# Optimization experiments

Measured on AMD Instinct MI355X. Metric: run time of the kernel, lower is better.

## Reference

```python
import jax, jax.numpy as jnp
import numpy as np

E = 1024          # embd_size
HS = 64           # head_size
NH = E // HS      # num heads = 16
B, T = 2, 2048


def setup_inputs() -> dict:
    key = jax.random.key(0)
    ks = jax.random.split(key, 9)
    s = 1.0 / np.sqrt(E)
    inp = {
        "embd_q": jax.random.normal(ks[0], (B, T, E), dtype=jnp.float32),
        # torch nn.Linear weights are [out, in]; y = x @ W.T + b
        "Wq": jax.random.uniform(ks[1], (E, E), jnp.float32, -s, s),
        "bq": jax.random.uniform(ks[2], (E,), jnp.float32, -s, s),
        "Wk": jax.random.uniform(ks[3], (E, E), jnp.float32, -s, s),
        "bk": jax.random.uniform(ks[4], (E,), jnp.float32, -s, s),
        "Wv": jax.random.uniform(ks[5], (E, E), jnp.float32, -s, s),
        "bv": jax.random.uniform(ks[6], (E,), jnp.float32, -s, s),
        "Wo": jax.random.uniform(ks[7], (E, E), jnp.float32, -s, s),
        "bo": jax.random.uniform(ks[8], (E,), jnp.float32, -s, s),
    }
    return inp


def reference(embd_q, Wq, bq, Wk, bk, Wv, bv, Wo, bo):
    b, t, e = embd_q.shape
    q = embd_q @ Wq.T + bq
    k = embd_q @ Wk.T + bk
    v = embd_q @ Wv.T + bv
    # [B, NH, T, HS]
    q = q.reshape(b, t, NH, HS).transpose(0, 2, 1, 3)
    k = k.reshape(b, t, NH, HS).transpose(0, 2, 1, 3)
    v = v.reshape(b, t, NH, HS).transpose(0, 2, 1, 3)
    w = jnp.einsum("bhqd,bhkd->bhqk", q, k) / jnp.sqrt(jnp.float32(HS))
    causal = jnp.triu(jnp.ones((t, t), dtype=bool), k=1)  # True above diag
    w = jnp.where(causal[None, None, :, :], -jnp.inf, w)
    w = jax.nn.softmax(w, axis=-1)
    a = jnp.einsum("bhqk,bhkd->bhqd", w, v)
    a = a.transpose(0, 2, 1, 3).reshape(b, t, e)
    return a @ Wo.T + bo
```

## Files before the change

### kernel.cpp

```cpp
#include <hip/hip_runtime.h>

typedef unsigned short u16;
typedef __bf16 bf16x8 __attribute__((ext_vector_type(8)));
typedef __bf16 bf16x4 __attribute__((ext_vector_type(4)));
typedef __bf16 bf16x2 __attribute__((ext_vector_type(2)));
typedef short s16x4 __attribute__((ext_vector_type(4)));
typedef float f32x4 __attribute__((ext_vector_type(4)));

#define Mdim 4096
#define Ndim 1024
#define Kdim 1024

__device__ __forceinline__ u16 f2bf(float f) {
    unsigned u = __float_as_uint(f);
    u += 0x7FFF + ((u >> 16) & 1);
    return (u16)(u >> 16);
}

__device__ __forceinline__ void gl_lds16(const u16* g, u16* l) {
    __builtin_amdgcn_global_load_lds(
        (const __attribute__((address_space(1))) unsigned int*)g,
        (__attribute__((address_space(3))) unsigned int*)l, 16, 0, 0);
}

__device__ __forceinline__ f32x4 mfma16(s16x4 a, s16x4 b, f32x4 c) {
#if __has_builtin(__builtin_amdgcn_mfma_f32_16x16x16_bf16)
    return __builtin_amdgcn_mfma_f32_16x16x16_bf16(
        __builtin_bit_cast(bf16x4, a), __builtin_bit_cast(bf16x4, b), c, 0, 0, 0);
#else
    return __builtin_amdgcn_mfma_f32_16x16x16bf16_1k(a, b, c, 0, 0, 0);
#endif
}

#if __has_builtin(__builtin_amdgcn_exp2f)
#define EXP2(x) __builtin_amdgcn_exp2f(x)
#else
#define EXP2(x) exp2f(x)
#endif

__device__ __forceinline__ s16x4 pack4bf(float a, float b, float c, float d) {
#if __has_builtin(__builtin_amdgcn_cvt_pk_bf16_f32)
    union { struct { bf16x2 lo, hi; } v; s16x4 s; } u;
    u.v.lo = __builtin_amdgcn_cvt_pk_bf16_f32(a, b);
    u.v.hi = __builtin_amdgcn_cvt_pk_bf16_f32(c, d);
    return u.s;
#else
    s16x4 r;
    r.x = (short)f2bf(a); r.y = (short)f2bf(b);
    r.z = (short)f2bf(c); r.w = (short)f2bf(d);
    return r;
#endif
}

__global__ __launch_bounds__(256) void cast_all(
    const float* __restrict__ X,
    const float* __restrict__ Wq, const float* __restrict__ Wk,
    const float* __restrict__ Wv, const float* __restrict__ Wo,
    u16* __restrict__ Xb,
    u16* __restrict__ Wqb, u16* __restrict__ Wkb,
    u16* __restrict__ Wvb, u16* __restrict__ Wob) {
    size_t i4 = (size_t)blockIdx.x * blockDim.x + threadIdx.x;
    size_t flat = i4 * 4;
    const float* src;
    u16* dst;
    size_t off;
    if (flat < (size_t)4194304) {
        src = X; dst = Xb; off = flat;
    } else {
        size_t r = flat - 4194304;
        int w = (int)(r >> 20);
        off = r & 1048575;
        src = (w == 0) ? Wq : (w == 1) ? Wk : (w == 2) ? Wv : Wo;
        dst = (w == 0) ? Wqb : (w == 1) ? Wkb : (w == 2) ? Wvb : Wob;
    }
    float4 v = *(const float4*)(src + off);
    ushort4 o;
    o.x = f2bf(v.x); o.y = f2bf(v.y); o.z = f2bf(v.z); o.w = f2bf(v.w);
    *(ushort4*)(dst + off) = o;
}

template <int BN>
__device__ __forceinline__ void gemm_core(const u16* __restrict__ A,
                                          const u16* __restrict__ Bw,
                                          const float* __restrict__ bias,
                                          void* __restrict__ out,
                                          int n0, int mode) {
    __shared__ __align__(16) u16 At[128 * 64];
    __shared__ __align__(16) u16 Bt[BN * 64];
    const int tid = threadIdx.x, w = tid >> 6, lane = tid & 63;
    const int quad = lane >> 4, l16 = lane & 15;
    const int wm = w & 1, wn = w >> 1;
    const int m0 = blockIdx.x * 128;
    constexpr int NTN = BN / 32;
    f32x4 acc[4][NTN] = {};
    const int r8 = lane >> 3, c8 = lane & 7;

    for (int k0 = 0; k0 < Kdim; k0 += 64) {
        __syncthreads();
#pragma unroll
        for (int i = 0; i < 4; ++i) {
            int row = w * 32 + i * 8 + r8;
            int j = c8 ^ (row & 7);
            gl_lds16(A + (size_t)(m0 + row) * Kdim + k0 + j * 8,
                     &At[(w * 32 + i * 8) * 64]);
        }
#pragma unroll
        for (int i = 0; i < BN / 32; ++i) {
            int row = w * (BN / 4) + i * 8 + r8;
            int j = c8 ^ (row & 7);
            gl_lds16(Bw + (size_t)(n0 + row) * Kdim + k0 + j * 8,
                     &Bt[(w * (BN / 4) + i * 8) * 64]);
        }
        __syncthreads();
#pragma unroll
        for (int ks = 0; ks < 2; ++ks) {
            bf16x8 af[4], bf[NTN];
#pragma unroll
            for (int mt = 0; mt < 4; ++mt) {
                int r = wm * 64 + mt * 16 + l16;
                af[mt] = *(const bf16x8*)&At[r * 64 + ((ks * 4 + quad) ^ (r & 7)) * 8];
            }
#pragma unroll
            for (int nt = 0; nt < NTN; ++nt) {
                int r = wn * (BN / 2) + nt * 16 + l16;
                bf[nt] = *(const bf16x8*)&Bt[r * 64 + ((ks * 4 + quad) ^ (r & 7)) * 8];
            }
#pragma unroll
            for (int mt = 0; mt < 4; ++mt)
#pragma unroll
                for (int nt = 0; nt < NTN; ++nt)
                    acc[mt][nt] = __builtin_amdgcn_mfma_f32_16x16x32_bf16(
                        af[mt], bf[nt], acc[mt][nt], 0, 0, 0);
        }
    }

#pragma unroll
    for (int nt = 0; nt < NTN; ++nt) {
        int n = n0 + wn * (BN / 2) + nt * 16 + l16;
        float bb = bias[n];
        const int h = n >> 6, d = n & 63;
        const int ksf = (d >> 5) & 1, quadf8 = (d >> 3) & 3, jj = d & 7;
        const int dtf = d >> 4, l16f = d & 15;
#pragma unroll
        for (int mt = 0; mt < 4; ++mt) {
            int mbase = m0 + wm * 64 + mt * 16 + quad * 4;
            if (mode == 2) {
                int b = mbase >> 11, t = mbase & 2047;
                int kt = t >> 5, kl = t & 31;
                int c = kl >> 4, quadf = (kl >> 2) & 3;
                ushort4 pk;
                pk.x = f2bf(acc[mt][nt][0] + bb);
                pk.y = f2bf(acc[mt][nt][1] + bb);
                pk.z = f2bf(acc[mt][nt][2] + bb);
                pk.w = f2bf(acc[mt][nt][3] + bb);
                *(ushort4*)&((u16*)out)[(size_t)(b * 16 + h) * 131072 + kt * 2048 +
                                        (c * 4 + dtf) * 256 + (quadf * 16 + l16f) * 4] = pk;
            } else if (mode == 3 || mode == 4) {
#pragma unroll
                for (int r = 0; r < 4; ++r) {
                    int m = mbase + r;
                    int b = m >> 11, t = m & 2047;
                    int blk = t >> 5, tl = t & 31;
                    int cq = tl >> 4, l16q = tl & 15;
                    ((u16*)out)[(size_t)(b * 16 + h) * 131072 + blk * 2048 +
                                (cq * 2 + ksf) * 512 + (quadf8 * 16 + l16q) * 8 + jj] =
                        f2bf(acc[mt][nt][r] + bb);
                }
            } else {
#pragma unroll
                for (int r = 0; r < 4; ++r)
                    ((float*)out)[(size_t)(mbase + r) * Ndim + n] = acc[mt][nt][r] + bb;
            }
        }
    }
}

__global__ __launch_bounds__(256, 2) void qkv_gemm(
    const u16* __restrict__ Xb,
    const u16* __restrict__ Wqb, const u16* __restrict__ Wkb, const u16* __restrict__ Wvb,
    const float* __restrict__ bq, const float* __restrict__ bk, const float* __restrict__ bv,
    u16* __restrict__ Qw, u16* __restrict__ Kw, u16* __restrict__ Vw) {
    const int y = blockIdx.y;
    const int z = y >> 3;
    const int n0 = (y & 7) * 128;
    const u16* Bw = (z == 0) ? Wqb : (z == 1) ? Wkb : Wvb;
    const float* bias = (z == 0) ? bq : (z == 1) ? bk : bv;
    void* out = (z == 0) ? (void*)Qw : (z == 1) ? (void*)Kw : (void*)Vw;
    gemm_core<128>(Xb, Bw, bias, out, n0, (z == 0) ? 3 : (z == 1) ? 4 : 2);
}

__global__ __launch_bounds__(256, 2) void out_gemm(
    const u16* __restrict__ Aatt, const u16* __restrict__ Wob,
    const float* __restrict__ bo, float* __restrict__ out) {
    gemm_core<64>(Aatt, Wob, bo, out, blockIdx.y * 64, 1);
}

__global__ __launch_bounds__(256, 3) void flash_attn(
    const u16* __restrict__ QF, const u16* __restrict__ KF,
    const u16* __restrict__ VF, u16* __restrict__ Aatt) {
    __shared__ float oLds[4 * 2112];
    __shared__ float lsumLds[4][32];

    const int tid = threadIdx.x, w = tid >> 6, lane = tid & 63;
    const int quad = lane >> 4, l16 = lane & 15;
    const int g = blockIdx.x;
    const int bh = g & 31;
    const int strip = 63 - (g >> 5);
    const int qbase = strip * 32;
    const int ntw = strip + 1;

    const u16* QFh = QF + (size_t)bh * 131072;
    const u16* KFh = KF + (size_t)bh * 131072;
    const u16* VFh = VF + (size_t)bh * 131072;
    const int b = bh >> 4, h = bh & 15;
    const float c1 = 0.18033688011112042f;

    bf16x8 qf[2][2];
#pragma unroll
    for (int qt = 0; qt < 2; ++qt)
#pragma unroll
        for (int ks = 0; ks < 2; ++ks)
            qf[qt][ks] = *(const bf16x8*)(QFh + (size_t)strip * 2048 +
                                          (qt * 2 + ks) * 512 + lane * 8);

    f32x4 o[2][4] = {};
    float lsum[2] = {0.f, 0.f};

#define LOADT(kt_, ka_, vf_)                                                   \
    {                                                                          \
        const u16* kp_ = KFh + (size_t)(kt_) * 2048;                           \
        const u16* vp_ = VFh + (size_t)(kt_) * 2048;                           \
        _Pragma("unroll")                                                      \
        for (int c_ = 0; c_ < 2; ++c_) {                                       \
            _Pragma("unroll")                                                  \
            for (int ks_ = 0; ks_ < 2; ++ks_)                                  \
                ka_[c_][ks_] = *(const bf16x8*)(kp_ + (c_ * 2 + ks_) * 512     \
                                                + lane * 8);                   \
            _Pragma("unroll")                                                  \
            for (int dt_ = 0; dt_ < 4; ++dt_)                                  \
                vf_[c_][dt_] = *(const s16x4*)(vp_ + (c_ * 4 + dt_) * 256      \
                                               + lane * 4);                    \
        }                                                                      \
    }

#define COMPUTE(kt_, ka_, vf_)                                                 \
    {                                                                          \
        const bool dm_ = ((kt_) == ntw - 1);                                   \
        _Pragma("unroll")                                                      \
        for (int c_ = 0; c_ < 2; ++c_) {                                       \
            _Pragma("unroll")                                                  \
            for (int qt_ = 0; qt_ < 2; ++qt_) {                                \
                f32x4 z_ = {};                                                 \
                z_ = __builtin_amdgcn_mfma_f32_16x16x32_bf16(                  \
                    ka_[c_][0], qf[qt_][0], z_, 0, 0, 0);                      \
                z_ = __builtin_amdgcn_mfma_f32_16x16x32_bf16(                  \
                    ka_[c_][1], qf[qt_][1], z_, 0, 0, 0);                      \
                float p_[4];                                                   \
                if (dm_) {                                                     \
                    int q_ = qbase + qt_ * 16 + l16;                           \
                    int kkb_ = (kt_) * 32 + c_ * 16 + quad * 4;                \
                    _Pragma("unroll")                                          \
                    for (int r_ = 0; r_ < 4; ++r_)                             \
                        p_[r_] = (kkb_ + r_ > q_) ? 0.f : EXP2(z_[r_] * c1);   \
                } else {                                                       \
                    _Pragma("unroll")                                          \
                    for (int r_ = 0; r_ < 4; ++r_) p_[r_] = EXP2(z_[r_] * c1); \
                }                                                              \
                lsum[qt_] += (p_[0] + p_[1]) + (p_[2] + p_[3]);                \
                s16x4 pa_ = pack4bf(p_[0], p_[1], p_[2], p_[3]);               \
                _Pragma("unroll")                                              \
                for (int dt_ = 0; dt_ < 4; ++dt_)                              \
                    o[qt_][dt_] = mfma16(pa_, vf_[c_][dt_], o[qt_][dt_]);      \
            }                                                                  \
        }                                                                      \
    }

    bf16x8 kaA[2][2], kaB[2][2];
    s16x4 vfA[2][4], vfB[2][4];
    int kt = w;
    if (kt < ntw) {
        LOADT(kt, kaA, vfA);
        while (true) {
            int nx = kt + 4;
            if (nx < ntw) {
                LOADT(nx, kaB, vfB);
                asm volatile("s_waitcnt vmcnt(12)" ::: "memory");
            } else {
                asm volatile("s_waitcnt vmcnt(0)" ::: "memory");
            }
            COMPUTE(kt, kaA, vfA);
            kt = nx;
            if (kt >= ntw) break;
            nx = kt + 4;
            if (nx < ntw) {
                LOADT(nx, kaA, vfA);
                asm volatile("s_waitcnt vmcnt(12)" ::: "memory");
            } else {
                asm volatile("s_waitcnt vmcnt(0)" ::: "memory");
            }
            COMPUTE(kt, kaB, vfB);
            kt = nx;
            if (kt >= ntw) break;
        }
    }

#pragma unroll
    for (int qt = 0; qt < 2; ++qt) {
        float l = lsum[qt];
        l += __shfl_xor(l, 16);
        l += __shfl_xor(l, 32);
        if (lane < 16) lsumLds[w][qt * 16 + lane] = l;
#pragma unroll
        for (int dt = 0; dt < 4; ++dt)
#pragma unroll
            for (int r = 0; r < 4; ++r)
                oLds[w * 2112 + (qt * 16 + quad * 4 + r) * 66 + dt * 16 + l16] =
                    o[qt][dt][r];
    }
    __syncthreads();
    {
        const int q = tid >> 3, dd = (tid & 7) * 8;
        float l = lsumLds[0][q] + lsumLds[1][q] + lsumLds[2][q] + lsumLds[3][q];
        float inv = 1.0f / l;
        f32x4 a0 = {}, a1 = {};
#pragma unroll
        for (int ww = 0; ww < 4; ++ww) {
            a0 += *(const f32x4*)&oLds[ww * 2112 + q * 66 + dd];
            a1 += *(const f32x4*)&oLds[ww * 2112 + q * 66 + dd + 4];
        }
        const int t = qbase + q;
        ushort4 p0, p1;
        p0.x = f2bf(a0[0] * inv); p0.y = f2bf(a0[1] * inv);
        p0.z = f2bf(a0[2] * inv); p0.w = f2bf(a0[3] * inv);
        p1.x = f2bf(a1[0] * inv); p1.y = f2bf(a1[1] * inv);
        p1.z = f2bf(a1[2] * inv); p1.w = f2bf(a1[3] * inv);
        u16* dst = Aatt + ((size_t)(b * 2048 + t)) * 1024 + h * 64 + dd;
        *(ushort4*)dst = p0;
        *(ushort4*)(dst + 4) = p1;
    }
}

extern "C" void kernel_launch(void* const* d_in, const int* in_sizes, int n_in,
                              void* d_out, int out_size, void* d_ws, size_t ws_size,
                              hipStream_t stream) {
    const float* X  = (const float*)d_in[0];
    const float* Wq = (const float*)d_in[1];
    const float* bq = (const float*)d_in[2];
    const float* Wk = (const float*)d_in[3];
    const float* bk = (const float*)d_in[4];
    const float* Wv = (const float*)d_in[5];
    const float* bv = (const float*)d_in[6];
    const float* Wo = (const float*)d_in[7];
    const float* bo = (const float*)d_in[8];

    char* ws = (char*)d_ws;
    const size_t MB = 1 << 20;
    u16* Xb   = (u16*)(ws);
    u16* Wqb  = (u16*)(ws + 8  * MB);
    u16* Wkb  = (u16*)(ws + 10 * MB);
    u16* Wvb  = (u16*)(ws + 12 * MB);
    u16* Wob  = (u16*)(ws + 14 * MB);
    u16* Qw   = (u16*)(ws + 16 * MB);
    u16* Kw   = (u16*)(ws + 24 * MB);
    u16* Vw   = (u16*)(ws + 32 * MB);
    u16* Aatt = (u16*)(ws + 40 * MB);

    cast_all<<<8192, 256, 0, stream>>>(X, Wq, Wk, Wv, Wo, Xb, Wqb, Wkb, Wvb, Wob);
    qkv_gemm<<<dim3(32, 24), 256, 0, stream>>>(Xb, Wqb, Wkb, Wvb, bq, bk, bv, Qw, Kw, Vw);
    flash_attn<<<dim3(2048), 256, 0, stream>>>(Qw, Kw, Vw, Aatt);
    out_gemm<<<dim3(32, 16), 256, 0, stream>>>(Aatt, Wob, bo, (float*)d_out);
}
```

Baseline: 167.4 us.

## Pre-swizzle operands into MFMA fragment layout and give each attention wave its own strip

The cast kernel now writes X, Wq, Wk and Wv directly in MFMA fragment order, so the QKV GEMM loads fragments straight from global memory into registers with double buffering and no LDS or barriers. Flash attention changes from four waves splitting the key tiles of one query strip (reduced through LDS) to each wave owning a separate query strip over all its keys. This removes the cross-wave reduction and shrinks the grid from 2048 to 512 blocks. The cost is that causal work is uneven across the four waves of a block, and output stores become scalar 16-bit writes.

Result: slower. 190.0 us (+13.4%).

```diff
diff --git a/kernel.cpp b/kernel.cpp
--- a/kernel.cpp
+++ b/kernel.cpp
@@ -52,91 +52,105 @@
 #endif
 }
 
-__global__ __launch_bounds__(256) void cast_all(
+__global__ __launch_bounds__(256) void cast_swz(
     const float* __restrict__ X,
     const float* __restrict__ Wq, const float* __restrict__ Wk,
     const float* __restrict__ Wv, const float* __restrict__ Wo,
-    u16* __restrict__ Xb,
-    u16* __restrict__ Wqb, u16* __restrict__ Wkb,
-    u16* __restrict__ Wvb, u16* __restrict__ Wob) {
-    size_t i4 = (size_t)blockIdx.x * blockDim.x + threadIdx.x;
-    size_t flat = i4 * 4;
+    u16* __restrict__ Xf,
+    u16* __restrict__ Wqf, u16* __restrict__ Wkf,
+    u16* __restrict__ Wvf, u16* __restrict__ Wob) {
+    size_t flat = ((size_t)blockIdx.x * 256 + threadIdx.x) * 8;
     const float* src;
     u16* dst;
-    size_t off;
-    if (flat < (size_t)4194304) {
-        src = X; dst = Xb; off = flat;
+    size_t soff;
+    int row = 0, col = 0;
+    bool frag;
+    if (flat < 4194304) {
+        src = X; dst = Xf; soff = flat;
+        row = (int)(flat >> 10); col = (int)(flat & 1023); frag = true;
     } else {
         size_t r = flat - 4194304;
-        int w = (int)(r >> 20);
-        off = r & 1048575;
-        src = (w == 0) ? Wq : (w == 1) ? Wk : (w == 2) ? Wv : Wo;
-        dst = (w == 0) ? Wqb : (w == 1) ? Wkb : (w == 2) ? Wvb : Wob;
-    }
-    float4 v = *(const float4*)(src + off);
-    ushort4 o;
-    o.x = f2bf(v.x); o.y = f2bf(v.y); o.z = f2bf(v.z); o.w = f2bf(v.w);
-    *(ushort4*)(dst + off) = o;
-}
-
-template <int BN>
-__device__ __forceinline__ void gemm_core(const u16* __restrict__ A,
-                                          const u16* __restrict__ Bw,
-                                          const float* __restrict__ bias,
-                                          void* __restrict__ out,
-                                          int n0, int mode) {
-    __shared__ __align__(16) u16 At[128 * 64];
-    __shared__ __align__(16) u16 Bt[BN * 64];
+        if (r < 3145728) {
+            int wsel = (int)(r >> 20);
+            soff = r & 1048575;
+            src = (wsel == 0) ? Wq : (wsel == 1) ? Wk : Wv;
+            dst = (wsel == 0) ? Wqf : (wsel == 1) ? Wkf : Wvf;
+            row = (int)(soff >> 10); col = (int)(soff & 1023); frag = true;
+        } else {
+            soff = r - 3145728;
+            src = Wo; dst = Wob; frag = false;
+        }
+    }
+    float4 v0 = *(const float4*)(src + soff);
+    float4 v1 = *(const float4*)(src + soff + 4);
+    u16 t[8];
+    t[0] = f2bf(v0.x); t[1] = f2bf(v0.y); t[2] = f2bf(v0.z); t[3] = f2bf(v0.w);
+    t[4] = f2bf(v1.x); t[5] = f2bf(v1.y); t[6] = f2bf(v1.z); t[7] = f2bf(v1.w);
+    size_t doff = frag
+        ? ((((size_t)(row >> 4) * 32 + (col >> 5)) * 4 + ((col >> 3) & 3)) * 128
+           + (size_t)(row & 15) * 8)
+        : soff;
+    *(uint4*)(dst + doff) = *(uint4*)t;
+}
+
+__global__ __launch_bounds__(256, 3) void qkv_gemm(
+    const u16* __restrict__ Xf,
+    const u16* __restrict__ Wqf, const u16* __restrict__ Wkf, const u16* __restrict__ Wvf,
+    const float* __restrict__ bq, const float* __restrict__ bk, const float* __restrict__ bv,
+    u16* __restrict__ Qw, u16* __restrict__ Kw, u16* __restrict__ Vw) {
+    const int y = blockIdx.y;
+    const int z = y >> 3;
+    const int n0 = (y & 7) * 128;
+    const u16* Wf = (z == 0) ? Wqf : (z == 1) ? Wkf : Wvf;
+    const float* bias = (z == 0) ? bq : (z == 1) ? bk : bv;
+
     const int tid = threadIdx.x, w = tid >> 6, lane = tid & 63;
     const int quad = lane >> 4, l16 = lane & 15;
     const int wm = w & 1, wn = w >> 1;
     const int m0 = blockIdx.x * 128;
-    constexpr int NTN = BN / 32;
-    f32x4 acc[4][NTN] = {};
-    const int r8 = lane >> 3, c8 = lane & 7;
-
-    for (int k0 = 0; k0 < Kdim; k0 += 64) {
-        __syncthreads();
-#pragma unroll
-        for (int i = 0; i < 4; ++i) {
-            int row = w * 32 + i * 8 + r8;
-            int j = c8 ^ (row & 7);
-            gl_lds16(A + (size_t)(m0 + row) * Kdim + k0 + j * 8,
-                     &At[(w * 32 + i * 8) * 64]);
-        }
-#pragma unroll
-        for (int i = 0; i < BN / 32; ++i) {
-            int row = w * (BN / 4) + i * 8 + r8;
-            int j = c8 ^ (row & 7);
-            gl_lds16(Bw + (size_t)(n0 + row) * Kdim + k0 + j * 8,
-                     &Bt[(w * (BN / 4) + i * 8) * 64]);
-        }
-        __syncthreads();
-#pragma unroll
-        for (int ks = 0; ks < 2; ++ks) {
-            bf16x8 af[4], bf[NTN];
-#pragma unroll
-            for (int mt = 0; mt < 4; ++mt) {
-                int r = wm * 64 + mt * 16 + l16;
-                af[mt] = *(const bf16x8*)&At[r * 64 + ((ks * 4 + quad) ^ (r & 7)) * 8];
-            }
-#pragma unroll
-            for (int nt = 0; nt < NTN; ++nt) {
-                int r = wn * (BN / 2) + nt * 16 + l16;
-                bf[nt] = *(const bf16x8*)&Bt[r * 64 + ((ks * 4 + quad) ^ (r & 7)) * 8];
-            }
-#pragma unroll
-            for (int mt = 0; mt < 4; ++mt)
-#pragma unroll
-                for (int nt = 0; nt < NTN; ++nt)
-                    acc[mt][nt] = __builtin_amdgcn_mfma_f32_16x16x32_bf16(
-                        af[mt], bf[nt], acc[mt][nt], 0, 0, 0);
-        }
-    }
-
-#pragma unroll
-    for (int nt = 0; nt < NTN; ++nt) {
-        int n = n0 + wn * (BN / 2) + nt * 16 + l16;
+
+    const u16* Af = Xf + ((size_t)(m0 >> 4) + wm * 4) * 16384;
+    const u16* Bf = Wf + ((size_t)(n0 >> 4) + wn * 4) * 16384;
+
+    f32x4 acc[4][4] = {};
+    bf16x8 aA[4], bA[4], aB[4], bB[4];
+
+#define QLOAD(kt_, a_, b_)                                                     \
+    {                                                                          \
+        _Pragma("unroll")                                                      \
+        for (int i_ = 0; i_ < 4; ++i_) {                                       \
+            a_[i_] = *(const bf16x8*)(Af + ((size_t)i_ * 32 + (kt_)) * 512 + lane * 8); \
+            b_[i_] = *(const bf16x8*)(Bf + ((size_t)i_ * 32 + (kt_)) * 512 + lane * 8); \
+        }                                                                      \
+    }
+#define QCOMP(a_, b_)                                                          \
+    {                                                                          \
+        _Pragma("unroll")                                                      \
+        for (int mt_ = 0; mt_ < 4; ++mt_)                                      \
+            _Pragma("unroll")                                                  \
+            for (int nt_ = 0; nt_ < 4; ++nt_)                                  \
+                acc[mt_][nt_] = __builtin_amdgcn_mfma_f32_16x16x32_bf16(       \
+                    a_[mt_], b_[nt_], acc[mt_][nt_], 0, 0, 0);                 \
+    }
+
+    QLOAD(0, aA, bA);
+#pragma unroll 1
+    for (int kt = 0; kt < 32; kt += 2) {
+        QLOAD(kt + 1, aB, bB);
+        asm volatile("s_waitcnt vmcnt(8)" ::: "memory");
+        QCOMP(aA, bA);
+        if (kt + 2 < 32) {
+            QLOAD(kt + 2, aA, bA);
+            asm volatile("s_waitcnt vmcnt(8)" ::: "memory");
+        } else {
+            asm volatile("s_waitcnt vmcnt(0)" ::: "memory");
+        }
+        QCOMP(aB, bB);
+    }
+
+#pragma unroll
+    for (int nt = 0; nt < 4; ++nt) {
+        int n = n0 + wn * 64 + nt * 16 + l16;
         float bb = bias[n];
         const int h = n >> 6, d = n & 63;
         const int ksf = (d >> 5) & 1, quadf8 = (d >> 3) & 3, jj = d & 7;
@@ -144,7 +158,7 @@
 #pragma unroll
         for (int mt = 0; mt < 4; ++mt) {
             int mbase = m0 + wm * 64 + mt * 16 + quad * 4;
-            if (mode == 2) {
+            if (z == 2) {
                 int b = mbase >> 11, t = mbase & 2047;
                 int kt = t >> 5, kl = t & 31;
                 int c = kl >> 4, quadf = (kl >> 2) & 3;
@@ -153,59 +167,100 @@
                 pk.y = f2bf(acc[mt][nt][1] + bb);
                 pk.z = f2bf(acc[mt][nt][2] + bb);
                 pk.w = f2bf(acc[mt][nt][3] + bb);
-                *(ushort4*)&((u16*)out)[(size_t)(b * 16 + h) * 131072 + kt * 2048 +
-                                        (c * 4 + dtf) * 256 + (quadf * 16 + l16f) * 4] = pk;
-            } else if (mode == 3 || mode == 4) {
+                *(ushort4*)&Vw[(size_t)(b * 16 + h) * 131072 + kt * 2048 +
+                               (c * 4 + dtf) * 256 + (quadf * 16 + l16f) * 4] = pk;
+            } else {
+                u16* out = (z == 0) ? Qw : Kw;
 #pragma unroll
                 for (int r = 0; r < 4; ++r) {
                     int m = mbase + r;
                     int b = m >> 11, t = m & 2047;
                     int blk = t >> 5, tl = t & 31;
                     int cq = tl >> 4, l16q = tl & 15;
-                    ((u16*)out)[(size_t)(b * 16 + h) * 131072 + blk * 2048 +
-                                (cq * 2 + ksf) * 512 + (quadf8 * 16 + l16q) * 8 + jj] =
+                    out[(size_t)(b * 16 + h) * 131072 + blk * 2048 +
+                        (cq * 2 + ksf) * 512 + (quadf8 * 16 + l16q) * 8 + jj] =
                         f2bf(acc[mt][nt][r] + bb);
                 }
-            } else {
-#pragma unroll
-                for (int r = 0; r < 4; ++r)
-                    ((float*)out)[(size_t)(mbase + r) * Ndim + n] = acc[mt][nt][r] + bb;
-            }
-        }
-    }
-}
-
-__global__ __launch_bounds__(256, 2) void qkv_gemm(
-    const u16* __restrict__ Xb,
-    const u16* __restrict__ Wqb, const u16* __restrict__ Wkb, const u16* __restrict__ Wvb,
-    const float* __restrict__ bq, const float* __restrict__ bk, const float* __restrict__ bv,
-    u16* __restrict__ Qw, u16* __restrict__ Kw, u16* __restrict__ Vw) {
-    const int y = blockIdx.y;
-    const int z = y >> 3;
-    const int n0 = (y & 7) * 128;
-    const u16* Bw = (z == 0) ? Wqb : (z == 1) ? Wkb : Wvb;
-    const float* bias = (z == 0) ? bq : (z == 1) ? bk : bv;
-    void* out = (z == 0) ? (void*)Qw : (z == 1) ? (void*)Kw : (void*)Vw;
-    gemm_core<128>(Xb, Bw, bias, out, n0, (z == 0) ? 3 : (z == 1) ? 4 : 2);
+            }
+        }
+    }
 }
 
 __global__ __launch_bounds__(256, 2) void out_gemm(
-    const u16* __restrict__ Aatt, const u16* __restrict__ Wob,
-    const float* __restrict__ bo, float* __restrict__ out) {
-    gemm_core<64>(Aatt, Wob, bo, out, blockIdx.y * 64, 1);
-}
-
-__global__ __launch_bounds__(256, 3) void flash_attn(
+    const u16* __restrict__ A, const u16* __restrict__ Bw,
+    const float* __restrict__ bias, float* __restrict__ out) {
+    constexpr int BN = 64;
+    __shared__ __align__(16) u16 At[128 * 64];
+    __shared__ __align__(16) u16 Bt[BN * 64];
+    const int tid = threadIdx.x, w = tid >> 6, lane = tid & 63;
+    const int quad = lane >> 4, l16 = lane & 15;
+    const int wm = w & 1, wn = w >> 1;
+    const int m0 = blockIdx.x * 128, n0 = blockIdx.y * BN;
+    constexpr int NTN = BN / 32;
+    f32x4 acc[4][NTN] = {};
+    const int r8 = lane >> 3, c8 = lane & 7;
+
+    for (int k0 = 0; k0 < Kdim; k0 += 64) {
+        __syncthreads();
+#pragma unroll
+        for (int i = 0; i < 4; ++i) {
+            int row = w * 32 + i * 8 + r8;
+            int j = c8 ^ (row & 7);
+            gl_lds16(A + (size_t)(m0 + row) * Kdim + k0 + j * 8,
+                     &At[(w * 32 + i * 8) * 64]);
+        }
+#pragma unroll
+        for (int i = 0; i < BN / 32; ++i) {
+            int row = w * (BN / 4) + i * 8 + r8;
+            int j = c8 ^ (row & 7);
+            gl_lds16(Bw + (size_t)(n0 + row) * Kdim + k0 + j * 8,
+                     &Bt[(w * (BN / 4) + i * 8) * 64]);
+        }
+        __syncthreads();
+#pragma unroll
+        for (int ks = 0; ks < 2; ++ks) {
+            bf16x8 af[4], bf[NTN];
+#pragma unroll
+            for (int mt = 0; mt < 4; ++mt) {
+                int r = wm * 64 + mt * 16 + l16;
+                af[mt] = *(const bf16x8*)&At[r * 64 + ((ks * 4 + quad) ^ (r & 7)) * 8];
+            }
+#pragma unroll
+            for (int nt = 0; nt < NTN; ++nt) {
+                int r = wn * (BN / 2) + nt * 16 + l16;
+                bf[nt] = *(const bf16x8*)&Bt[r * 64 + ((ks * 4 + quad) ^ (r & 7)) * 8];
+            }
+#pragma unroll
+            for (int mt = 0; mt < 4; ++mt)
+#pragma unroll
+                for (int nt = 0; nt < NTN; ++nt)
+                    acc[mt][nt] = __builtin_amdgcn_mfma_f32_16x16x32_bf16(
+                        af[mt], bf[nt], acc[mt][nt], 0, 0, 0);
+        }
+    }
+#pragma unroll
+    for (int nt = 0; nt < NTN; ++nt) {
+        int n = n0 + wn * (BN / 2) + nt * 16 + l16;
+        float bb = bias[n];
+#pragma unroll
+        for (int mt = 0; mt < 4; ++mt) {
+            int mbase = m0 + wm * 64 + mt * 16 + quad * 4;
+#pragma unroll
+            for (int r = 0; r < 4; ++r)
+                out[(size_t)(mbase + r) * Ndim + n] = acc[mt][nt][r] + bb;
+        }
+    }
+}
+
+__global__ __launch_bounds__(256, 2) void flash_attn(
     const u16* __restrict__ QF, const u16* __restrict__ KF,
     const u16* __restrict__ VF, u16* __restrict__ Aatt) {
-    __shared__ float oLds[4 * 2112];
-    __shared__ float lsumLds[4][32];
-
     const int tid = threadIdx.x, w = tid >> 6, lane = tid & 63;
     const int quad = lane >> 4, l16 = lane & 15;
     const int g = blockIdx.x;
     const int bh = g & 31;
-    const int strip = 63 - (g >> 5);
+    const int sg = g >> 5;
+    const int strip = (15 - sg) * 4 + w;
     const int qbase = strip * 32;
     const int ntw = strip + 1;
 
@@ -277,29 +332,28 @@
 
     bf16x8 kaA[2][2], kaB[2][2];
     s16x4 vfA[2][4], vfB[2][4];
-    int kt = w;
-    if (kt < ntw) {
-        LOADT(kt, kaA, vfA);
+    {
+        int kt = 0;
+        LOADT(0, kaA, vfA);
+#pragma unroll 1
         while (true) {
-            int nx = kt + 4;
-            if (nx < ntw) {
-                LOADT(nx, kaB, vfB);
+            if (kt + 1 < ntw) {
+                LOADT(kt + 1, kaB, vfB);
                 asm volatile("s_waitcnt vmcnt(12)" ::: "memory");
             } else {
                 asm volatile("s_waitcnt vmcnt(0)" ::: "memory");
             }
             COMPUTE(kt, kaA, vfA);
-            kt = nx;
+            ++kt;
             if (kt >= ntw) break;
-            nx = kt + 4;
-            if (nx < ntw) {
-                LOADT(nx, kaA, vfA);
+            if (kt + 1 < ntw) {
+                LOADT(kt + 1, kaA, vfA);
                 asm volatile("s_waitcnt vmcnt(12)" ::: "memory");
             } else {
                 asm volatile("s_waitcnt vmcnt(0)" ::: "memory");
             }
             COMPUTE(kt, kaB, vfB);
-            kt = nx;
+            ++kt;
             if (kt >= ntw) break;
         }
     }
@@ -309,34 +363,20 @@
         float l = lsum[qt];
         l += __shfl_xor(l, 16);
         l += __shfl_xor(l, 32);
-        if (lane < 16) lsumLds[w][qt * 16 + lane] = l;
-#pragma unroll
-        for (int dt = 0; dt < 4; ++dt)
-#pragma unroll
-            for (int r = 0; r < 4; ++r)
-                oLds[w * 2112 + (qt * 16 + quad * 4 + r) * 66 + dt * 16 + l16] =
-                    o[qt][dt][r];
-    }
-    __syncthreads();
-    {
-        const int q = tid >> 3, dd = (tid & 7) * 8;
-        float l = lsumLds[0][q] + lsumLds[1][q] + lsumLds[2][q] + lsumLds[3][q];
         float inv = 1.0f / l;
-        f32x4 a0 = {}, a1 = {};
-#pragma unroll
-        for (int ww = 0; ww < 4; ++ww) {
-            a0 += *(const f32x4*)&oLds[ww * 2112 + q * 66 + dd];
-            a1 += *(const f32x4*)&oLds[ww * 2112 + q * 66 + dd + 4];
-        }
-        const int t = qbase + q;
-        ushort4 p0, p1;
-        p0.x = f2bf(a0[0] * inv); p0.y = f2bf(a0[1] * inv);
-        p0.z = f2bf(a0[2] * inv); p0.w = f2bf(a0[3] * inv);
-        p1.x = f2bf(a1[0] * inv); p1.y = f2bf(a1[1] * inv);
-        p1.z = f2bf(a1[2] * inv); p1.w = f2bf(a1[3] * inv);
-        u16* dst = Aatt + ((size_t)(b * 2048 + t)) * 1024 + h * 64 + dd;
-        *(ushort4*)dst = p0;
-        *(ushort4*)(dst + 4) = p1;
+        float rinv[4];
+#pragma unroll
+        for (int r = 0; r < 4; ++r)
+            rinv[r] = __shfl(inv, (lane & 48) + quad * 4 + r);
+#pragma unroll
+        for (int dt = 0; dt < 4; ++dt) {
+            int e = h * 64 + dt * 16 + l16;
+#pragma unroll
+            for (int r = 0; r < 4; ++r) {
+                int t = qbase + qt * 16 + quad * 4 + r;
+                Aatt[((size_t)(b * 2048 + t)) * 1024 + e] = f2bf(o[qt][dt][r] * rinv[r]);
+            }
+        }
     }
 }
 
@@ -355,18 +395,18 @@
 
     char* ws = (char*)d_ws;
     const size_t MB = 1 << 20;
-    u16* Xb   = (u16*)(ws);
-    u16* Wqb  = (u16*)(ws + 8  * MB);
-    u16* Wkb  = (u16*)(ws + 10 * MB);
-    u16* Wvb  = (u16*)(ws + 12 * MB);
+    u16* Xf   = (u16*)(ws);
+    u16* Wqf  = (u16*)(ws + 8  * MB);
+    u16* Wkf  = (u16*)(ws + 10 * MB);
+    u16* Wvf  = (u16*)(ws + 12 * MB);
     u16* Wob  = (u16*)(ws + 14 * MB);
     u16* Qw   = (u16*)(ws + 16 * MB);
     u16* Kw   = (u16*)(ws + 24 * MB);
     u16* Vw   = (u16*)(ws + 32 * MB);
     u16* Aatt = (u16*)(ws + 40 * MB);
 
-    cast_all<<<8192, 256, 0, stream>>>(X, Wq, Wk, Wv, Wo, Xb, Wqb, Wkb, Wvb, Wob);
-    qkv_gemm<<<dim3(32, 24), 256, 0, stream>>>(Xb, Wqb, Wkb, Wvb, bq, bk, bv, Qw, Kw, Vw);
-    flash_attn<<<dim3(2048), 256, 0, stream>>>(Qw, Kw, Vw, Aatt);
+    cast_swz<<<4096, 256, 0, stream>>>(X, Wq, Wk, Wv, Wo, Xf, Wqf, Wkf, Wvf, Wob);
+    qkv_gemm<<<dim3(32, 24), 256, 0, stream>>>(Xf, Wqf, Wkf, Wvf, bq, bk, bv, Qw, Kw, Vw);
+    flash_attn<<<dim3(512), 256, 0, stream>>>(Qw, Kw, Vw, Aatt);
     out_gemm<<<dim3(32, 16), 256, 0, stream>>>(Aatt, Wob, bo, (float*)d_out);
 }
```
